# Kernel optimization log

Measured on AMD Instinct MI355X. Metric: run time of the kernel, lower is better.

## Reference

```python
import jax, jax.numpy as jnp
import numpy as np

NEG_SLOPE = 0.2
EPS = 1e-16


def gat_conv(x, edge_index, W, att_src, att_dst, bias, heads, out_ch, concat):
    """PyG GATConv (eval mode, add_self_loops=True).
    x: [N, F_in], edge_index: [2, E] with row0=src(j), row1=dst(i).
    W: [F_in, heads*out_ch], att_src/att_dst: [heads, out_ch], bias: [heads*out_ch] or [out_ch].
    """
    N = x.shape[0]
    loop = jnp.arange(N, dtype=edge_index.dtype)
    src = jnp.concatenate([edge_index[0], loop])
    dst = jnp.concatenate([edge_index[1], loop])

    h = (x @ W).reshape(N, heads, out_ch)                 # [N, H, C]
    a_src = jnp.sum(h * att_src[None], axis=-1)           # [N, H]
    a_dst = jnp.sum(h * att_dst[None], axis=-1)           # [N, H]

    alpha = jax.nn.leaky_relu(a_src[src] + a_dst[dst], NEG_SLOPE)  # [E, H]
    # segment softmax over incoming edges of each destination node
    m = jax.ops.segment_max(alpha, dst, num_segments=N)   # [N, H]
    e = jnp.exp(alpha - m[dst])                           # [E, H]
    s = jax.ops.segment_sum(e, dst, num_segments=N)       # [N, H]
    alpha = e / (s[dst] + EPS)                            # [E, H]

    out = jax.ops.segment_sum(h[src] * alpha[:, :, None], dst, num_segments=N)  # [N, H, C]
    if concat:
        out = out.reshape(N, heads * out_ch)
    else:
        out = out.mean(axis=1)
    return out + bias


def setup_inputs() -> dict:
    key = jax.random.key(0)
    ks = jax.random.split(key, 12)
    N, E, F_in, C = 100000, 1600000, 512, 16
    H1, O1 = 8, 8
    hid = H1 * O1  # 64
    sc1 = 1.0 / np.sqrt(F_in)
    sc2 = 1.0 / np.sqrt(hid)
    return {
        "x": jax.random.normal(ks[0], (N, F_in), jnp.float32),
        "edge_index": jax.random.randint(ks[1], (2, E), 0, N, jnp.int64),
        "W1": jax.random.normal(ks[2], (F_in, hid), jnp.float32) * sc1,
        "att_src1": jax.random.normal(ks[3], (H1, O1), jnp.float32) * sc2,
        "att_dst1": jax.random.normal(ks[4], (H1, O1), jnp.float32) * sc2,
        "bias1": jnp.zeros((hid,), jnp.float32),
        "W2": jax.random.normal(ks[5], (hid, C), jnp.float32) * sc2,
        "att_src2": jax.random.normal(ks[6], (1, C), jnp.float32) * 0.25,
        "att_dst2": jax.random.normal(ks[7], (1, C), jnp.float32) * 0.25,
        "bias2": jnp.zeros((C,), jnp.float32),
    }


def reference(x, edge_index, W1, att_src1, att_dst1, bias1, W2, att_src2, att_dst2, bias2):
    h = gat_conv(x, edge_index, W1, att_src1, att_dst1, bias1, heads=8, out_ch=8, concat=True)
    h = jax.nn.elu(h)
    C = W2.shape[1]
    node_embeddings = gat_conv(h, edge_index, W2, att_src2, att_dst2, bias2, heads=1, out_ch=C, concat=True)
    out = jax.nn.softmax(node_embeddings, axis=-1)
    return (out, node_embeddings)
```

## Files before the change

### kernel.cpp

```cpp
#include <hip/hip_runtime.h>
#include <hip/hip_bf16.h>

#define NEG_SLOPE 0.2f
#define EPSF 1e-16f

typedef __attribute__((ext_vector_type(8))) short bf16x8;
typedef __attribute__((ext_vector_type(4))) float f32x4;

__device__ inline unsigned short f2bf(float x) {
  unsigned int u = __float_as_uint(x);
  return (unsigned short)((u + 0x7fffu + ((u >> 16) & 1u)) >> 16);
}
__device__ inline float bf2f(unsigned short h) {
  return __uint_as_float(((unsigned int)h) << 16);
}

__device__ __forceinline__ void gload16(const void* src, void* dst) {
  __builtin_amdgcn_global_load_lds(
      (const __attribute__((address_space(1))) unsigned int*)src,
      (__attribute__((address_space(3))) unsigned int*)dst, 16, 0, 0);
}

__global__ __launch_bounds__(256) void prep_count_kernel(const float* __restrict__ W,
                                                         unsigned short* __restrict__ wb,
                                                         int* __restrict__ deg,
                                                         const int* __restrict__ ei, int E) {
  const int b = blockIdx.x, tid = threadIdx.x;
  if (b < 128) {
    int idx = b * 256 + tid;
    int k = idx >> 6, c = idx & 63;
    float w = W[idx];
    unsigned short h = f2bf(w);
    unsigned short l = f2bf(w - bf2f(h));
    int ch = k >> 5, kin = k & 31;
    int Ap = ((c << 6) + (kin << 1)) ^ ((c & 7) << 4);
    wb[ch * 4096 + (Ap >> 1)] = h;
    wb[ch * 4096 + 2048 + (Ap >> 1)] = l;
  } else {
    int e = (b - 128) * 256 + tid;
    if (e < E) atomicAdd(&deg[ei[E + e]], 1);
  }
}

__global__ __launch_bounds__(256) void scan1_kernel(int* __restrict__ data, int* __restrict__ blocksum, int N) {
  __shared__ int wave_tot[4];
  int t = threadIdx.x;
  int base = blockIdx.x * 1024;
  int v[4];
  int sum = 0;
#pragma unroll
  for (int i = 0; i < 4; ++i) {
    int idx = base + t * 4 + i;
    v[i] = sum;
    int d = (idx < N) ? data[idx] : 0;
    sum += d;
  }
  int lane = t & 63, wv = t >> 6;
  int x = sum;
#pragma unroll
  for (int ofs = 1; ofs < 64; ofs <<= 1) {
    int y = __shfl_up(x, ofs);
    if (lane >= ofs) x += y;
  }
  if (lane == 63) wave_tot[wv] = x;
  __syncthreads();
  int wofs = 0;
  for (int w = 0; w < wv; ++w) wofs += wave_tot[w];
  int excl_thread = wofs + x - sum;
#pragma unroll
  for (int i = 0; i < 4; ++i) {
    int idx = base + t * 4 + i;
    if (idx < N) data[idx] = excl_thread + v[i];
  }
  if (t == 255) blocksum[blockIdx.x] = wofs + x;
}

__global__ __launch_bounds__(256) void scan2_kernel(int* __restrict__ blocksum, int nb) {
  __shared__ int sm[256];
  int t = threadIdx.x;
  int x = (t < nb) ? blocksum[t] : 0;
  sm[t] = x;
  __syncthreads();
  for (int ofs = 1; ofs < 256; ofs <<= 1) {
    int y = (t >= ofs) ? sm[t - ofs] : 0;
    __syncthreads();
    sm[t] += y;
    __syncthreads();
  }
  if (t < nb) blocksum[t] = sm[t] - x;
}

__global__ __launch_bounds__(256) void scan3_kernel(const int* __restrict__ excl, const int* __restrict__ blocksum,
                                                    int* __restrict__ rowptr, int* __restrict__ cursor,
                                                    int N, int ET) {
  int idx = blockIdx.x * 256 + threadIdx.x;
  if (idx < N) {
    int r = excl[idx] + blocksum[idx >> 10] + idx;
    rowptr[idx] = r;
    cursor[idx] = r;
  }
  if (idx == N) rowptr[N] = ET;
}

__global__ __launch_bounds__(256) void scatter_kernel(const int* __restrict__ ei, int E, int ET,
                                                      int* __restrict__ cursor, int* __restrict__ esrc, int N) {
  const int cls = blockIdx.x & 7;
  const int nlo = (int)(((long long)N * cls) >> 3);
  const int nhi = (int)(((long long)N * (cls + 1)) >> 3);
  const int chunk = blockIdx.x >> 3;
  const int nchunks = gridDim.x >> 3;
  const long long stride = (long long)nchunks * 256;
  for (long long e = (long long)chunk * 256 + threadIdx.x; e < ET; e += stride) {
    int d = (e < E) ? ei[E + e] : (int)(e - E);
    if (d >= nlo && d < nhi) {
      int s = (e < E) ? ei[e] : d;
      int pos = atomicAdd(&cursor[d], 1);
      esrc[pos] = s;
    }
  }
}

__global__ __launch_bounds__(256) void gemm1_kernel(const float* __restrict__ x,
                                                    const unsigned short* __restrict__ wb,
                                                    const float* __restrict__ atts,
                                                    const float* __restrict__ attd,
                                                    unsigned short* __restrict__ h1b,
                                                    float* __restrict__ a1s,
                                                    float* __restrict__ a1d, int N) {
  __shared__ __align__(16) float As[3][4096];
  __shared__ __align__(16) unsigned short Bs[3][4096];
  const int tid = threadIdx.x, wv = tid >> 6, lane = tid & 63;
  const int row0 = blockIdx.x * 128;

  const float* asrc[4];
  int aldo[4];
#pragma unroll
  for (int i = 0; i < 4; ++i) {
    int u = i * 256 + wv * 64 + lane;
    int row = u >> 3, w = u & 7;
    int rg = row0 + row;
    if (rg >= N) rg = N - 1;
    asrc[i] = x + (size_t)rg * 512 + ((w ^ (row & 7)) << 2);
    aldo[i] = (i * 256 + wv * 64) * 4;
  }
  const unsigned short* bsrc[2];
  int bldo[2];
#pragma unroll
  for (int i = 0; i < 2; ++i) {
    int u = i * 256 + wv * 64 + lane;
    bsrc[i] = wb + (size_t)u * 8;
    bldo[i] = (i * 256 + wv * 64) * 8;
  }

  const int kofs = (lane >> 4) * 8;
  const int cbase = lane & 15;
  int ardo[2][2];
#pragma unroll
  for (int rt = 0; rt < 2; ++rt) {
    int r = wv * 32 + rt * 16 + cbase;
#pragma unroll
    for (int h = 0; h < 2; ++h)
      ardo[rt][h] = r * 32 + ((((kofs >> 2) + h) ^ (r & 7)) << 2);
  }
  int brdo[4];
#pragma unroll
  for (int ct = 0; ct < 4; ++ct) {
    int c = ct * 16 + cbase;
    brdo[ct] = (((c << 6) + (kofs << 1)) ^ ((c & 7) << 4)) >> 1;
  }

  f32x4 acc[2][4] = {};

  auto stage = [&](int b, int ch) {
#pragma unroll
    for (int i = 0; i < 4; ++i) gload16(asrc[i] + ch * 32, &As[b][aldo[i]]);
#pragma unroll
    for (int i = 0; i < 2; ++i) gload16(bsrc[i] + ch * 4096, &Bs[b][bldo[i]]);
  };

  stage(0, 0);
  stage(1, 1);
  for (int i = 0; i < 16; ++i) {
    const int b = i % 3;
    if (i < 14) {
      stage((i + 2) % 3, i + 2);
      asm volatile("s_waitcnt vmcnt(12)" ::: "memory");
    } else if (i == 14) {
      asm volatile("s_waitcnt vmcnt(6)" ::: "memory");
    } else {
      asm volatile("s_waitcnt vmcnt(0)" ::: "memory");
    }
    __builtin_amdgcn_s_barrier();
    __builtin_amdgcn_sched_barrier(0);

#pragma unroll
    for (int rt = 0; rt < 2; ++rt) {
      float4 a0 = *(const float4*)(&As[b][ardo[rt][0]]);
      float4 a1 = *(const float4*)(&As[b][ardo[rt][1]]);
      float av[8] = {a0.x, a0.y, a0.z, a0.w, a1.x, a1.y, a1.z, a1.w};
      bf16x8 ah, al;
#pragma unroll
      for (int j = 0; j < 8; ++j) {
        unsigned int u = __float_as_uint(av[j]);
        ah[j] = (short)(unsigned short)(u >> 16);
        float lo = av[j] - __uint_as_float(u & 0xffff0000u);
        al[j] = (short)(unsigned short)(__float_as_uint(lo) >> 16);
      }
#pragma unroll
      for (int ct = 0; ct < 4; ++ct) {
        bf16x8 bh = *(const bf16x8*)(&Bs[b][brdo[ct]]);
        bf16x8 bl = *(const bf16x8*)(&Bs[b][brdo[ct] + 2048]);
        acc[rt][ct] = __builtin_amdgcn_mfma_f32_16x16x32_bf16(ah, bh, acc[rt][ct], 0, 0, 0);
        acc[rt][ct] = __builtin_amdgcn_mfma_f32_16x16x32_bf16(al, bh, acc[rt][ct], 0, 0, 0);
        acc[rt][ct] = __builtin_amdgcn_mfma_f32_16x16x32_bf16(ah, bl, acc[rt][ct], 0, 0, 0);
      }
    }
    asm volatile("s_waitcnt lgkmcnt(0)" ::: "memory");
    __builtin_amdgcn_s_barrier();
  }

  float wS[4], wD[4];
#pragma unroll
  for (int ct = 0; ct < 4; ++ct) {
    wS[ct] = atts[ct * 16 + cbase];
    wD[ct] = attd[ct * 16 + cbase];
  }
#pragma unroll
  for (int rt = 0; rt < 2; ++rt) {
#pragma unroll
    for (int ct = 0; ct < 4; ++ct) {
#pragma unroll
      for (int j = 0; j < 4; ++j) {
        int r = row0 + wv * 32 + rt * 16 + (lane >> 4) * 4 + j;
        float a = acc[rt][ct][j];
        if (r < N) h1b[(size_t)r * 64 + ct * 16 + cbase] = f2bf(a);
        float ps = a * wS[ct], pd = a * wD[ct];
        ps += __shfl_xor(ps, 1); pd += __shfl_xor(pd, 1);
        ps += __shfl_xor(ps, 2); pd += __shfl_xor(pd, 2);
        ps += __shfl_xor(ps, 4); pd += __shfl_xor(pd, 4);
        if ((lane & 7) == 0 && r < N) {
          int h = ct * 2 + ((lane >> 3) & 1);
          a1s[r * 8 + h] = ps;
          a1d[r * 8 + h] = pd;
        }
      }
    }
  }
}

__global__ __launch_bounds__(256) void agg1_kernel(const int* __restrict__ rowptr, const int* __restrict__ esrc,
                                                   const float* __restrict__ a1s, const float* __restrict__ a1d,
                                                   const unsigned short* __restrict__ h1b,
                                                   const float* __restrict__ bias1,
                                                   unsigned short* __restrict__ h2b, int N) {
  const int wid = (blockIdx.x * 256 + threadIdx.x) >> 6;
  const int lane = threadIdx.x & 63;
  const int q = lane >> 4, l = lane & 15;
  const int nA = wid * 4;
  if (nA >= N) return;
  const int n = nA + q;
  const bool nvalid = n < N;
  const int nc = nvalid ? n : nA;
  const int h = l >> 1;
  const int c4 = l * 4;

  const float ad = a1d[(unsigned)nc * 8 + h];
  const int beg = rowptr[nc];
  const int deg = nvalid ? (rowptr[nc + 1] - beg) : 0;
  int dm = max(deg, __shfl_xor(deg, 16));
  dm = max(dm, __shfl_xor(dm, 32));
  const int dcl = max(deg, 1) - 1;

  float acc0 = 0.f, acc1 = 0.f, acc2 = 0.f, acc3 = 0.f, wsum = 0.f;
  for (int it = 0; it < dm; it += 2) {
    int k0 = beg + min(it, dcl);
    int k1 = beg + min(it + 1, dcl);
    float m0 = (it < deg) ? 1.f : 0.f;
    float m1 = (it + 1 < deg) ? 1.f : 0.f;
    int s0 = esrc[k0], s1 = esrc[k1];
    uint2 g0 = *(const uint2*)(h1b + ((unsigned)s0 * 64 + c4));
    uint2 g1 = *(const uint2*)(h1b + ((unsigned)s1 * 64 + c4));
    float al0 = a1s[(unsigned)s0 * 8 + h] + ad;
    float al1 = a1s[(unsigned)s1 * 8 + h] + ad;
    al0 = fmaxf(al0, NEG_SLOPE * al0);
    al1 = fmaxf(al1, NEG_SLOPE * al1);
    float w0 = __expf(al0) * m0;
    float w1 = __expf(al1) * m1;
    acc0 = fmaf(w0, bf2f((unsigned short)(g0.x & 0xffff)), acc0);
    acc1 = fmaf(w0, bf2f((unsigned short)(g0.x >> 16)), acc1);
    acc2 = fmaf(w0, bf2f((unsigned short)(g0.y & 0xffff)), acc2);
    acc3 = fmaf(w0, bf2f((unsigned short)(g0.y >> 16)), acc3);
    acc0 = fmaf(w1, bf2f((unsigned short)(g1.x & 0xffff)), acc0);
    acc1 = fmaf(w1, bf2f((unsigned short)(g1.x >> 16)), acc1);
    acc2 = fmaf(w1, bf2f((unsigned short)(g1.y & 0xffff)), acc2);
    acc3 = fmaf(w1, bf2f((unsigned short)(g1.y >> 16)), acc3);
    wsum += w0 + w1;
  }
  float inv = 1.f / (wsum + EPSF);
  float4 b4 = *(const float4*)(bias1 + c4);
  float v0 = acc0 * inv + b4.x;
  float v1 = acc1 * inv + b4.y;
  float v2 = acc2 * inv + b4.z;
  float v3 = acc3 * inv + b4.w;
  v0 = (v0 > 0.f) ? v0 : expm1f(v0);
  v1 = (v1 > 0.f) ? v1 : expm1f(v1);
  v2 = (v2 > 0.f) ? v2 : expm1f(v2);
  v3 = (v3 > 0.f) ? v3 : expm1f(v3);
  if (nvalid) {
    uint2 pack;
    pack.x = (unsigned int)f2bf(v0) | ((unsigned int)f2bf(v1) << 16);
    pack.y = (unsigned int)f2bf(v2) | ((unsigned int)f2bf(v3) << 16);
    *(uint2*)(h2b + ((unsigned)n * 64 + c4)) = pack;
  }
}

__global__ __launch_bounds__(256) void l2_proj_kernel(const unsigned short* __restrict__ h2b,
                                                      const float* __restrict__ W2,
                                                      const float* __restrict__ atts, const float* __restrict__ attd,
                                                      unsigned short* __restrict__ gb, float* __restrict__ a2s,
                                                      float* __restrict__ a2d, int N) {
  __shared__ float w[1024];
  int tid = threadIdx.x;
  for (int i = tid; i < 1024; i += 256) w[i] = W2[i];
  __syncthreads();
  int gid = blockIdx.x * 256 + tid;
  int n = gid >> 4, c = gid & 15;
  if (n >= N) return;
  const unsigned short* hr = h2b + (size_t)n * 64;
  float acc = 0.f;
#pragma unroll
  for (int k8 = 0; k8 < 8; ++k8) {
    bf16x8 hv = *(const bf16x8*)(hr + k8 * 8);
#pragma unroll
    for (int j = 0; j < 8; ++j)
      acc = fmaf(bf2f((unsigned short)hv[j]), w[(k8 * 8 + j) * 16 + c], acc);
  }
  gb[(size_t)n * 16 + c] = f2bf(acc);
  float ps = acc * atts[c], pd = acc * attd[c];
#pragma unroll
  for (int m = 1; m < 16; m <<= 1) { ps += __shfl_xor(ps, m); pd += __shfl_xor(pd, m); }
  if (c == 0) { a2s[n] = ps; a2d[n] = pd; }
}

__global__ __launch_bounds__(256) void agg2_kernel(const int* __restrict__ rowptr, const int* __restrict__ esrc,
                                                   const float* __restrict__ a2s, const float* __restrict__ a2d,
                                                   const unsigned short* __restrict__ gb,
                                                   const float* __restrict__ bias2,
                                                   float* __restrict__ out_sm, float* __restrict__ emb, int N) {
  const int wid = (blockIdx.x * 256 + threadIdx.x) >> 6;
  const int lane = threadIdx.x & 63;
  const int q = lane >> 4, c = lane & 15;
  const int nA = wid * 4;
  if (nA >= N) return;
  const int n = nA + q;
  const bool nvalid = n < N;
  const int nc = nvalid ? n : nA;

  const float ad = a2d[nc];
  const int beg = rowptr[nc];
  const int deg = nvalid ? (rowptr[nc + 1] - beg) : 0;
  int dm = max(deg, __shfl_xor(deg, 16));
  dm = max(dm, __shfl_xor(dm, 32));
  const int dcl = max(deg, 1) - 1;

  float acc = 0.f, wsum = 0.f;
  for (int it = 0; it < dm; it += 2) {
    int k0 = beg + min(it, dcl);
    int k1 = beg + min(it + 1, dcl);
    float m0 = (it < deg) ? 1.f : 0.f;
    float m1 = (it + 1 < deg) ? 1.f : 0.f;
    int s0 = esrc[k0], s1 = esrc[k1];
    float al0 = a2s[s0] + ad;
    float al1 = a2s[s1] + ad;
    al0 = fmaxf(al0, NEG_SLOPE * al0);
    al1 = fmaxf(al1, NEG_SLOPE * al1);
    float w0 = __expf(al0) * m0;
    float w1 = __expf(al1) * m1;
    acc = fmaf(w0, bf2f(gb[(unsigned)s0 * 16 + c]), acc);
    acc = fmaf(w1, bf2f(gb[(unsigned)s1 * 16 + c]), acc);
    wsum += w0 + w1;
  }
  float v = acc / (wsum + EPSF) + bias2[c];
  float mx = v;
#pragma unroll
  for (int k2 = 1; k2 < 16; k2 <<= 1) mx = fmaxf(mx, __shfl_xor(mx, k2));
  float e = __expf(v - mx);
  float ssum = e;
#pragma unroll
  for (int k2 = 1; k2 < 16; k2 <<= 1) ssum += __shfl_xor(ssum, k2);
  if (nvalid) {
    emb[(size_t)n * 16 + c] = v;
    out_sm[(size_t)n * 16 + c] = e / ssum;
  }
}

extern "C" void kernel_launch(void* const* d_in, const int* in_sizes, int n_in,
                              void* d_out, int out_size, void* d_ws, size_t ws_size,
                              hipStream_t stream) {
  const float* x     = (const float*)d_in[0];
  const int*   ei    = (const int*)d_in[1];
  const float* W1    = (const float*)d_in[2];
  const float* atts1 = (const float*)d_in[3];
  const float* attd1 = (const float*)d_in[4];
  const float* bias1 = (const float*)d_in[5];
  const float* W2    = (const float*)d_in[6];
  const float* atts2 = (const float*)d_in[7];
  const float* attd2 = (const float*)d_in[8];
  const float* bias2 = (const float*)d_in[9];

  const int N = in_sizes[0] / 512;
  const int E = in_sizes[1] / 2;
  const int ET = E + N;

  char* wp = (char*)d_ws;
  unsigned short* h1b = (unsigned short*)wp;        wp += (size_t)N * 64 * 2;
  unsigned short* h2b = (unsigned short*)wp;        wp += (size_t)N * 64 * 2;
  float* a1s = (float*)wp;                          wp += (size_t)N * 8 * 4;
  float* a1d = (float*)wp;                          wp += (size_t)N * 8 * 4;
  unsigned short* gb = (unsigned short*)wp;         wp += (size_t)N * 16 * 2;
  float* a2s = (float*)wp;                          wp += (size_t)N * 4;
  float* a2d = (float*)wp;                          wp += (size_t)N * 4;
  int* deg = (int*)wp;                              wp += (size_t)N * 4;
  int* rowptr = (int*)wp;                           wp += (size_t)(N + 1) * 4;
  int* cursor = (int*)wp;                           wp += (size_t)N * 4;
  int* blocksum = (int*)wp;                         wp += 256 * 4;
  int* esrc = (int*)wp;                             wp += (size_t)ET * 4;
  unsigned short* wb = (unsigned short*)wp;         wp += 512 * 64 * 2 * 2;

  float* out_sm = (float*)d_out;
  float* emb    = out_sm + (size_t)N * 16;

  const int nb = (N + 1023) / 1024;
  const int nCnt = (E + 255) / 256;

  hipMemsetAsync(deg, 0, (size_t)N * sizeof(int), stream);
  prep_count_kernel<<<128 + nCnt, 256, 0, stream>>>(W1, wb, deg, ei, E);
  scan1_kernel<<<nb, 256, 0, stream>>>(deg, blocksum, N);
  scan2_kernel<<<1, 256, 0, stream>>>(blocksum, nb);
  scan3_kernel<<<(N + 256) / 256, 256, 0, stream>>>(deg, blocksum, rowptr, cursor, N, ET);
  scatter_kernel<<<8 * 1024, 256, 0, stream>>>(ei, E, ET, cursor, esrc, N);

  gemm1_kernel<<<(N + 127) / 128, 256, 0, stream>>>(x, wb, atts1, attd1, h1b, a1s, a1d, N);
  agg1_kernel<<<(N + 15) / 16, 256, 0, stream>>>(rowptr, esrc, a1s, a1d, h1b, bias1, h2b, N);

  l2_proj_kernel<<<(N * 16 + 255) / 256, 256, 0, stream>>>(h2b, W2, atts2, attd2, gb, a2s, a2d, N);
  agg2_kernel<<<(N + 15) / 16, 256, 0, stream>>>(rowptr, esrc, a2s, a2d, gb, bias2, out_sm, emb, N);
}
```

Baseline: 313.6 us.

## Fuse layer-2 projection into layer-1 aggregation and merge scan passes

The layer-2 projection (64x16 matmul plus attention dot products) now runs inside the layer-1 aggregation kernel. Each block stages its 16 aggregated rows in shared memory and projects them there, so the bf16 h2 intermediate is never written to or read back from global memory. Separately, the single-block blocksum scan is folded into the rowptr kernel, with every block redundantly scanning the block sums, which removes one launch. The risks are more shared memory per block in the aggregation kernel, a barrier that stalls until all waves finish their variable-length edge loops, and h2 now kept in fp32 rather than rounded to bf16.

```diff
diff --git a/kernel.cpp b/kernel.cpp
--- a/kernel.cpp
+++ b/kernel.cpp
@@ -75,27 +75,28 @@
   if (t == 255) blocksum[blockIdx.x] = wofs + x;
 }
 
-__global__ __launch_bounds__(256) void scan2_kernel(int* __restrict__ blocksum, int nb) {
-  __shared__ int sm[256];
+__global__ __launch_bounds__(256) void scan3_kernel(const int* __restrict__ excl,
+                                                    const int* __restrict__ blocksum, int nb,
+                                                    int* __restrict__ rowptr, int* __restrict__ cursor,
+                                                    int N, int ET) {
+  __shared__ int bs[256];
   int t = threadIdx.x;
   int x = (t < nb) ? blocksum[t] : 0;
-  sm[t] = x;
+  bs[t] = x;
   __syncthreads();
   for (int ofs = 1; ofs < 256; ofs <<= 1) {
-    int y = (t >= ofs) ? sm[t - ofs] : 0;
+    int y = (t >= ofs) ? bs[t - ofs] : 0;
     __syncthreads();
-    sm[t] += y;
+    bs[t] += y;
     __syncthreads();
   }
-  if (t < nb) blocksum[t] = sm[t] - x;
-}
-
-__global__ __launch_bounds__(256) void scan3_kernel(const int* __restrict__ excl, const int* __restrict__ blocksum,
-                                                    int* __restrict__ rowptr, int* __restrict__ cursor,
-                                                    int N, int ET) {
-  int idx = blockIdx.x * 256 + threadIdx.x;
+  int ex = bs[t] - x;
+  __syncthreads();
+  bs[t] = ex;
+  __syncthreads();
+  int idx = blockIdx.x * 256 + t;
   if (idx < N) {
-    int r = excl[idx] + blocksum[idx >> 10] + idx;
+    int r = excl[idx] + bs[idx >> 10] + idx;
     rowptr[idx] = r;
     cursor[idx] = r;
   }
@@ -248,22 +249,33 @@
   }
 }
 
-__global__ __launch_bounds__(256) void agg1_kernel(const int* __restrict__ rowptr, const int* __restrict__ esrc,
-                                                   const float* __restrict__ a1s, const float* __restrict__ a1d,
-                                                   const unsigned short* __restrict__ h1b,
-                                                   const float* __restrict__ bias1,
-                                                   unsigned short* __restrict__ h2b, int N) {
-  const int wid = (blockIdx.x * 256 + threadIdx.x) >> 6;
-  const int lane = threadIdx.x & 63;
+__global__ __launch_bounds__(256) void agg1_l2_kernel(const int* __restrict__ rowptr,
+                                                      const int* __restrict__ esrc,
+                                                      const float* __restrict__ a1s,
+                                                      const float* __restrict__ a1d,
+                                                      const unsigned short* __restrict__ h1b,
+                                                      const float* __restrict__ bias1,
+                                                      const float* __restrict__ W2,
+                                                      const float* __restrict__ atts2,
+                                                      const float* __restrict__ attd2,
+                                                      unsigned short* __restrict__ gb,
+                                                      float* __restrict__ a2s,
+                                                      float* __restrict__ a2d, int N) {
+  __shared__ float w2s[1024];
+  __shared__ float h2s[16][68];
+  const int tid = threadIdx.x;
+  const int wv = tid >> 6, lane = tid & 63;
   const int q = lane >> 4, l = lane & 15;
-  const int nA = wid * 4;
-  if (nA >= N) return;
-  const int n = nA + q;
+  const int nbase = blockIdx.x * 16;
+  const int nloc = wv * 4 + q;
+  const int n = nbase + nloc;
   const bool nvalid = n < N;
-  const int nc = nvalid ? n : nA;
+  const int nc = nvalid ? n : (N - 1);
+
+  for (int i = tid; i < 1024; i += 256) w2s[i] = W2[i];
+
   const int h = l >> 1;
   const int c4 = l * 4;
-
   const float ad = a1d[(unsigned)nc * 8 + h];
   const int beg = rowptr[nc];
   const int deg = nvalid ? (rowptr[nc + 1] - beg) : 0;
@@ -306,40 +318,26 @@
   v1 = (v1 > 0.f) ? v1 : expm1f(v1);
   v2 = (v2 > 0.f) ? v2 : expm1f(v2);
   v3 = (v3 > 0.f) ? v3 : expm1f(v3);
-  if (nvalid) {
-    uint2 pack;
-    pack.x = (unsigned int)f2bf(v0) | ((unsigned int)f2bf(v1) << 16);
-    pack.y = (unsigned int)f2bf(v2) | ((unsigned int)f2bf(v3) << 16);
-    *(uint2*)(h2b + ((unsigned)n * 64 + c4)) = pack;
-  }
-}
-
-__global__ __launch_bounds__(256) void l2_proj_kernel(const unsigned short* __restrict__ h2b,
-                                                      const float* __restrict__ W2,
-                                                      const float* __restrict__ atts, const float* __restrict__ attd,
-                                                      unsigned short* __restrict__ gb, float* __restrict__ a2s,
-                                                      float* __restrict__ a2d, int N) {
-  __shared__ float w[1024];
-  int tid = threadIdx.x;
-  for (int i = tid; i < 1024; i += 256) w[i] = W2[i];
+  h2s[nloc][c4 + 0] = v0;
+  h2s[nloc][c4 + 1] = v1;
+  h2s[nloc][c4 + 2] = v2;
+  h2s[nloc][c4 + 3] = v3;
   __syncthreads();
-  int gid = blockIdx.x * 256 + tid;
-  int n = gid >> 4, c = gid & 15;
-  if (n >= N) return;
-  const unsigned short* hr = h2b + (size_t)n * 64;
-  float acc = 0.f;
-#pragma unroll
-  for (int k8 = 0; k8 < 8; ++k8) {
-    bf16x8 hv = *(const bf16x8*)(hr + k8 * 8);
-#pragma unroll
-    for (int j = 0; j < 8; ++j)
-      acc = fmaf(bf2f((unsigned short)hv[j]), w[(k8 * 8 + j) * 16 + c], acc);
-  }
-  gb[(size_t)n * 16 + c] = f2bf(acc);
-  float ps = acc * atts[c], pd = acc * attd[c];
-#pragma unroll
-  for (int m = 1; m < 16; m <<= 1) { ps += __shfl_xor(ps, m); pd += __shfl_xor(pd, m); }
-  if (c == 0) { a2s[n] = ps; a2d[n] = pd; }
+
+  {
+    const int nl2 = tid >> 4, c = tid & 15;
+    const int n2 = nbase + nl2;
+    float acc = 0.f;
+#pragma unroll
+    for (int k = 0; k < 64; ++k) acc = fmaf(h2s[nl2][k], w2s[k * 16 + c], acc);
+    float ps = acc * atts2[c], pd = acc * attd2[c];
+#pragma unroll
+    for (int m = 1; m < 16; m <<= 1) { ps += __shfl_xor(ps, m); pd += __shfl_xor(pd, m); }
+    if (n2 < N) {
+      gb[(size_t)n2 * 16 + c] = f2bf(acc);
+      if (c == 0) { a2s[n2] = ps; a2d[n2] = pd; }
+    }
+  }
 }
 
 __global__ __launch_bounds__(256) void agg2_kernel(const int* __restrict__ rowptr, const int* __restrict__ esrc,
@@ -414,7 +412,6 @@
 
   char* wp = (char*)d_ws;
   unsigned short* h1b = (unsigned short*)wp;        wp += (size_t)N * 64 * 2;
-  unsigned short* h2b = (unsigned short*)wp;        wp += (size_t)N * 64 * 2;
   float* a1s = (float*)wp;                          wp += (size_t)N * 8 * 4;
   float* a1d = (float*)wp;                          wp += (size_t)N * 8 * 4;
   unsigned short* gb = (unsigned short*)wp;         wp += (size_t)N * 16 * 2;
@@ -436,13 +433,12 @@
   hipMemsetAsync(deg, 0, (size_t)N * sizeof(int), stream);
   prep_count_kernel<<<128 + nCnt, 256, 0, stream>>>(W1, wb, deg, ei, E);
   scan1_kernel<<<nb, 256, 0, stream>>>(deg, blocksum, N);
-  scan2_kernel<<<1, 256, 0, stream>>>(blocksum, nb);
-  scan3_kernel<<<(N + 256) / 256, 256, 0, stream>>>(deg, blocksum, rowptr, cursor, N, ET);
+  scan3_kernel<<<(N + 256) / 256, 256, 0, stream>>>(deg, blocksum, nb, rowptr, cursor, N, ET);
   scatter_kernel<<<8 * 1024, 256, 0, stream>>>(ei, E, ET, cursor, esrc, N);
 
   gemm1_kernel<<<(N + 127) / 128, 256, 0, stream>>>(x, wb, atts1, attd1, h1b, a1s, a1d, N);
-  agg1_kernel<<<(N + 15) / 16, 256, 0, stream>>>(rowptr, esrc, a1s, a1d, h1b, bias1, h2b, N);
-
-  l2_proj_kernel<<<(N * 16 + 255) / 256, 256, 0, stream>>>(h2b, W2, atts2, attd2, gb, a2s, a2d, N);
+  agg1_l2_kernel<<<(N + 15) / 16, 256, 0, stream>>>(rowptr, esrc, a1s, a1d, h1b, bias1,
+                                                    W2, atts2, attd2, gb, a2s, a2d, N);
+
   agg2_kernel<<<(N + 15) / 16, 256, 0, stream>>>(rowptr, esrc, a2s, a2d, gb, bias2, out_sm, emb, N);
 }
```

After: 304.0 us. -3.1%, faster.
